# Kernel tuning notes

Hardware: AMD Instinct MI355X
Metric: run time of the kernel (lower is better)

## Reference

```python
import jax, jax.numpy as jnp
import numpy as np

AT_ID = 5       # tokenizer id of '@'
CITSEG_ID = 7   # tokenizer id of 'CITSEG'


def setup_inputs() -> dict:
    key = jax.random.key(0)
    ks = jax.random.split(key, 12)
    B, S, H = 256, 512, 768
    CIT, D, NC = 750, 1518, 6
    s = lambda n: 1.0 / np.sqrt(n)
    return {
        "tokens": jax.random.randint(ks[0], (B, S), 0, 100),
        "hidden_states": jax.random.normal(ks[1], (B, S, H), jnp.float32),
        "proj_w": jax.random.normal(ks[2], (H, CIT), jnp.float32) * s(H),
        "proj_b": jax.random.normal(ks[3], (CIT,), jnp.float32) * 0.02,
        "enc_w": jax.random.normal(ks[4], (CIT, CIT), jnp.float32) * s(CIT),
        "enc_b": jax.random.normal(ks[5], (CIT,), jnp.float32) * 0.02,
        "w1": jax.random.normal(ks[6], (D, 2 * D), jnp.float32) * s(D),
        "b1": jax.random.normal(ks[7], (2 * D,), jnp.float32) * 0.02,
        "w2": jax.random.normal(ks[8], (2 * D, 2 * D), jnp.float32) * s(2 * D),
        "b2": jax.random.normal(ks[9], (2 * D,), jnp.float32) * 0.02,
        "w3": jax.random.normal(ks[10], (2 * D, NC), jnp.float32) * s(2 * D),
        "b3": jax.random.normal(ks[11], (NC,), jnp.float32) * 0.02,
    }


def _forward(tokens, hidden_states, proj_w, proj_b, enc_w, enc_b,
             w1, b1, w2, b2, w3, b3):
    B, S, H = hidden_states.shape
    idx = jnp.arange(S)[None, :]                       # [1,S]
    BIG = S + 1

    # --- ctx_pooler: masked max over tokens outside the [start,end] '@' span ---
    at_mask = tokens == AT_ID                          # [B,S]
    first = jnp.min(jnp.where(at_mask, idx, BIG), axis=1)            # [B]
    second = jnp.min(jnp.where(at_mask & (idx > first[:, None]), idx, BIG), axis=1)
    ge2 = at_mask.sum(axis=1) >= 2
    start = jnp.where(ge2, first, 0)
    end = jnp.where(ge2, second, S)                    # end=S excludes everything
    keep = (idx < start[:, None]) | (idx > end[:, None])             # [B,S]
    neg = jnp.finfo(hidden_states.dtype).min
    pooled = jnp.max(jnp.where(keep[:, :, None], hidden_states, neg), axis=1)  # [B,H]
    pooled = jnp.where(keep.any(axis=1)[:, None], pooled, 0.0)

    # --- CITSEG token gather + projection (zero row if absent) ---
    c_mask = tokens == CITSEG_ID
    c_first = jnp.min(jnp.where(c_mask, idx, BIG), axis=1)           # [B]
    has_c = c_mask.any(axis=1)
    safe_pos = jnp.minimum(c_first, S - 1)
    cit_h = jnp.take_along_axis(hidden_states, safe_pos[:, None, None], axis=1)[:, 0]  # [B,H]
    cit = (cit_h @ proj_w + proj_b) * has_c[:, None].astype(hidden_states.dtype)       # [B,750]

    # --- citseg_encoder (modeled as Linear 750->750) ---
    cit_enc = cit @ enc_w + enc_b

    # --- MLP head ---
    x = jnp.concatenate([pooled, cit_enc], axis=1)     # [B,1518]
    x = jax.nn.relu(x @ w1 + b1)
    x = jax.nn.relu(x @ w2 + b2)
    return x @ w3 + b3                                 # [B,num_class]


def reference(tokens, hidden_states, proj_w, proj_b, enc_w, enc_b,
              w1, b1, w2, b2, w3, b3):
    return _forward(tokens, hidden_states, proj_w, proj_b, enc_w, enc_b,
                    w1, b1, w2, b2, w3, b3)
```

## Files before the change

kernel.cpp:

```cpp
#include <hip/hip_runtime.h>
#include <hip/hip_bf16.h>

typedef __attribute__((ext_vector_type(8))) short bf16x8;
typedef __attribute__((ext_vector_type(4))) float f32x4;
typedef __attribute__((ext_vector_type(2))) float f32x2;
typedef __attribute__((ext_vector_type(4))) unsigned short u16x4;

#define NEGINF (-3.4028234663852886e38f)
#define BIGP (1 << 20)

__device__ __forceinline__ unsigned short f2b(float f) {
    union { float f; unsigned u; } x; x.f = f;
    unsigned r = x.u + 0x7FFFu + ((x.u >> 16) & 1u);
    return (unsigned short)(r >> 16);
}
__device__ __forceinline__ float b2f(unsigned short b) {
    union { unsigned u; float f; } x; x.u = ((unsigned)b) << 16;
    return x.f;
}
__device__ __forceinline__ void load_lds16(const void* g, void* l) {
    __builtin_amdgcn_global_load_lds((const __attribute__((address_space(1))) void*)g,
                                     (__attribute__((address_space(3))) void*)l, 16, 0, 0);
}
__device__ __forceinline__ int swzf(int r) { return (r & 15) ^ (r >> 4); }

#define GEMM_COMPUTE(as, bs)                                                        \
    _Pragma("unroll")                                                               \
    for (int ks = 0; ks < 4; ++ks) {                                                \
        int kc = ks * 4 + rsub;                                                     \
        bf16x8 af[2], bfr[2];                                                       \
        _Pragma("unroll")                                                           \
        for (int mi = 0; mi < 2; ++mi) {                                            \
            int rr = wr * 32 + mi * 16 + c_lin;                                     \
            af[mi] = *(const bf16x8*)((as) + rr * 128 + ((kc ^ c_lin ^ (wr * 2 + mi)) << 3)); \
        }                                                                           \
        _Pragma("unroll")                                                           \
        for (int nj = 0; nj < 2; ++nj) {                                            \
            int rr = wc * 32 + nj * 16 + c_lin;                                     \
            bfr[nj] = *(const bf16x8*)((bs) + rr * 128 + ((kc ^ c_lin ^ (wc * 2 + nj)) << 3)); \
        }                                                                           \
        _Pragma("unroll")                                                           \
        for (int mi = 0; mi < 2; ++mi)                                              \
            _Pragma("unroll")                                                       \
            for (int nj = 0; nj < 2; ++nj)                                          \
                acc[mi][nj] = __builtin_amdgcn_mfma_f32_16x16x32_bf16(              \
                    af[mi], bfr[nj], acc[mi][nj], 0, 0, 0);                         \
    }

__device__ __forceinline__ void wpe_body(const float* __restrict__ proj,
                                         const float* __restrict__ enc,
                                         unsigned short* __restrict__ WpeT,
                                         int bx, int by,
                                         unsigned short* AsB, unsigned short* BsB) {
    const int KR = 750;
    const int tid = threadIdx.x;
    const int wid = tid >> 6, lane = tid & 63;
    const int m0 = by * 64, n0 = bx * 64;
    const int wr = wid >> 1, wc = wid & 1;
    const int c_lin = lane & 15, rsub = lane >> 4;
    const int tn = (tid & 15) * 4, tc = tid >> 4;

    f32x4 acc[2][2];
    const f32x4 zero = {0.f, 0.f, 0.f, 0.f};
#pragma unroll
    for (int mi = 0; mi < 2; ++mi)
#pragma unroll
        for (int nj = 0; nj < 2; ++nj) acc[mi][nj] = zero;

    for (int t = 0; t < 6; ++t) {
        int kt = t << 7;
        float va[4][8];
#pragma unroll
        for (int p = 0; p < 4; ++p) {
            int r = m0 + p * 16 + tc;
#pragma unroll
            for (int e = 0; e < 4; ++e) {
                int d = kt + (tid & 15) * 8 + e * 2;
                int dcl = min(d, KR - 2);
                f32x2 t2 = *(const f32x2*)(proj + (size_t)r * KR + dcl);
                va[p][e * 2]     = (d < KR) ? t2[0] : 0.f;
                va[p][e * 2 + 1] = (d + 1 < KR) ? t2[1] : 0.f;
            }
        }
        f32x4 vb[8];
        int nbl = n0 + tn;
        int n1 = min(nbl, 748), n2 = min(nbl + 2, 748);
#pragma unroll
        for (int p = 0; p < 8; ++p) {
            int kg = min(kt + tc * 8 + p, KR - 1);
            const float* rowp = enc + (size_t)kg * KR;
            f32x2 a = *(const f32x2*)(rowp + n1);
            f32x2 b = *(const f32x2*)(rowp + n2);
            f32x4 tv; tv[0] = a[0]; tv[1] = a[1]; tv[2] = b[0]; tv[3] = b[1];
            vb[p] = tv;
        }
        __syncthreads();
#pragma unroll
        for (int p = 0; p < 4; ++p) {
            int r = p * 16 + tc;
            bf16x8 w;
#pragma unroll
            for (int e = 0; e < 8; ++e) w[e] = (short)f2b(va[p][e]);
            *(bf16x8*)(AsB + r * 128 + (((tid & 15) ^ swzf(r)) << 3)) = w;
        }
#pragma unroll
        for (int q = 0; q < 4; ++q) {
            int row = tn + q;
            bf16x8 w;
#pragma unroll
            for (int p = 0; p < 8; ++p) w[p] = (short)f2b(vb[p][q]);
            *(bf16x8*)(BsB + row * 128 + ((tc ^ swzf(row)) << 3)) = w;
        }
        __syncthreads();
        const unsigned short* as = AsB;
        const unsigned short* bs = BsB;
        GEMM_COMPUTE(as, bs)
    }
#pragma unroll
    for (int mi = 0; mi < 2; ++mi) {
        int hb = m0 + wr * 32 + mi * 16 + rsub * 4;
#pragma unroll
        for (int nj = 0; nj < 2; ++nj) {
            int j = n0 + wc * 32 + nj * 16 + c_lin;
#pragma unroll
            for (int i = 0; i < 4; ++i)
                WpeT[(size_t)j * 768 + hb + i] = f2b(acc[mi][nj][i]);
        }
    }
}

__device__ __forceinline__ void trans32(const float* __restrict__ in, int K, int N,
                                        unsigned short* __restrict__ out, int ldo,
                                        int bx, int by, int tid, float (*tile)[33]) {
    int n0 = bx * 32, k0 = by * 32;
    int tx = tid & 31, ty = tid >> 5;
#pragma unroll
    for (int i = 0; i < 4; ++i) {
        int k = k0 + ty * 4 + i, n = n0 + tx;
        tile[ty * 4 + i][tx] = (k < K && n < N) ? in[(size_t)k * N + n] : 0.f;
    }
    __syncthreads();
    int n = tid >> 3, kc = tid & 7;
    u16x4 o;
#pragma unroll
    for (int q = 0; q < 4; ++q) o[q] = f2b(tile[kc * 4 + q][n]);
    *(u16x4*)(out + (size_t)(n0 + n) * ldo + k0 + kc * 4) = o;
}

__global__ __launch_bounds__(256) void kA_k(
    const int* __restrict__ tokens, const float* __restrict__ hs,
    int* __restrict__ meta, unsigned short* __restrict__ citA,
    const float* __restrict__ proj_w, const float* __restrict__ enc_w,
    const float* __restrict__ proj_b, const float* __restrict__ enc_b,
    unsigned short* __restrict__ WpeT, float* __restrict__ bpe,
    float* __restrict__ part,
    const float* __restrict__ w1, const float* __restrict__ w2,
    unsigned short* __restrict__ w1T, unsigned short* __restrict__ w2T) {
    __shared__ __align__(16) char smem[32768];
    int bid = blockIdx.x, tid = threadIdx.x;
    if (bid < 64) {
        const int S = 512;
        int b = bid * 4 + (tid >> 6), l = tid & 63;
        const int* row = tokens + (size_t)b * S;
        int base = l * 8;
        int toks[8];
#pragma unroll
        for (int i = 0; i < 8; ++i) toks[i] = row[base + i];
        int am = 0, cnt = 0, minAt = BIGP, minC = BIGP;
#pragma unroll
        for (int i = 0; i < 8; ++i) {
            if (toks[i] == 5) { am |= 1 << i; cnt++; if (base + i < minAt) minAt = base + i; }
            if (toks[i] == 7) { if (base + i < minC) minC = base + i; }
        }
        for (int off = 1; off < 64; off <<= 1) {
            minAt = min(minAt, __shfl_xor(minAt, off));
            minC  = min(minC,  __shfl_xor(minC,  off));
            cnt  += __shfl_xor(cnt, off);
        }
        int first = minAt, minAt2 = BIGP;
#pragma unroll
        for (int i = 0; i < 8; ++i)
            if ((am >> i) & 1) { int idx = base + i; if (idx > first && idx < minAt2) minAt2 = idx; }
        for (int off = 1; off < 64; off <<= 1) minAt2 = min(minAt2, __shfl_xor(minAt2, off));
        if (l == 0) {
            int ge2 = (cnt >= 2) ? 1 : 0;
            int start = ge2 ? first : 0;
            int end = ge2 ? minAt2 : S;
            int anyKeep = (ge2 && (start > 0 || end < S - 1)) ? 1 : 0;
            int has_c = (minC < S) ? 1 : 0;
            int cpos = min(minC, S - 1);
            int* m = meta + b * 6;
            m[0] = start; m[1] = end; m[2] = cpos; m[3] = has_c; m[4] = anyKeep; m[5] = 0;
        }
        return;
    }
    if (bid < 320) {
        if (tid >= 192) return;
        int b = bid - 64, lane = tid & 63;
        const int* row = tokens + (size_t)b * 512;
        int minC = BIGP;
#pragma unroll
        for (int c = 0; c < 8; ++c) {
            int tok = row[c * 64 + lane];
            unsigned long long m = __ballot(tok == 7);
            if (minC == BIGP && m) minC = c * 64 + (int)__ffsll(m) - 1;
        }
        int cpos = min(minC, 511);
        f32x4 cv = *(const f32x4*)(hs + ((size_t)b * 512 + cpos) * 768 + tid * 4);
        u16x4 co;
#pragma unroll
        for (int j = 0; j < 4; ++j) co[j] = f2b(cv[j]);
        *(u16x4*)(citA + (size_t)b * 768 + tid * 4) = co;
        return;
    }
    if (bid < 464) {
        int r = bid - 320;
        wpe_body(proj_w, enc_w, WpeT, r % 12, r / 12,
                 (unsigned short*)smem, (unsigned short*)(smem + 16384));
        return;
    }
    if (bid < 467) {
        int j = (bid - 464) * 256 + tid;
        if (j < 750) {
            float a = enc_b[j];
            for (int d = 0; d < 750; ++d) a += proj_b[d] * enc_w[(size_t)d * 750 + j];
            bpe[j] = a;
        }
        return;
    }
    if (bid < 2515) {
        if (tid >= 192) return;
        int pb = bid - 467;
        int b = pb >> 3, ch = pb & 7;
        int lane = tid & 63;
        const int* row = tokens + (size_t)b * 512;
        int first = BIGP, second = BIGP;
#pragma unroll
        for (int c = 0; c < 8; ++c) {
            int tok = row[c * 64 + lane];
            unsigned long long m = __ballot(tok == 5);
            if (m) {
                int base = c * 64;
                if (first == BIGP) {
                    first = base + (int)__ffsll(m) - 1;
                    unsigned long long m2 = m & (m - 1);
                    if (m2) second = base + (int)__ffsll(m2) - 1;
                } else if (second == BIGP) {
                    second = base + (int)__ffsll(m) - 1;
                }
            }
        }
        int start, end;
        if (second < BIGP) { start = first; end = second; }
        else               { start = 0;     end = 512;    }
        f32x4 m = { NEGINF, NEGINF, NEGINF, NEGINF };
        const float* basep = hs + (size_t)b * 512 * 768 + tid * 4;
        int s0 = ch * 64, hi = s0 + 64;
        int e1 = min(start, hi);
        int s2 = max(end + 1, s0);
#pragma unroll 4
        for (int s = s0; s < e1; ++s) {
            f32x4 v = *(const f32x4*)(basep + (size_t)s * 768);
#pragma unroll
            for (int j = 0; j < 4; ++j) m[j] = fmaxf(m[j], v[j]);
        }
#pragma unroll 4
        for (int s = s2; s < hi; ++s) {
            f32x4 v = *(const f32x4*)(basep + (size_t)s * 768);
#pragma unroll
            for (int j = 0; j < 4; ++j) m[j] = fmaxf(m[j], v[j]);
        }
        *(f32x4*)(part + ((size_t)b * 8 + ch) * 768 + tid * 4) = m;
        return;
    }
    if (bid < 7123) {
        int r = bid - 2515;
        trans32(w1, 1518, 3036, w1T, 1536, r % 96, r / 96, tid, (float(*)[33])(void*)smem);
        return;
    }
    {
        int r = bid - 7123;
        trans32(w2, 3036, 3036, w2T, 3072, r % 96, r / 96, tid, (float(*)[33])(void*)smem);
    }
}

__device__ __forceinline__ void g12_body(
    const unsigned short* __restrict__ A, const unsigned short* __restrict__ Bt,
    const float* __restrict__ bpe, const float* __restrict__ encb,
    const int* __restrict__ meta, unsigned short* __restrict__ X,
    int bx, int by, unsigned short* AsB, unsigned short* BsB) {
    const int lda = 768, ldb = 768, ldx = 1536, Nreal = 750;
    const int tid = threadIdx.x;
    const int wid = tid >> 6, lane = tid & 63;
    const int m0 = by * 64, n0 = bx * 64;
    const int wr = wid >> 1, wc = wid & 1;
    const int c_lin = lane & 15, rsub = lane >> 4;

    int aoff[4], boff[4], ldst[4];
#pragma unroll
    for (int i = 0; i < 4; ++i) {
        int r = wid * 16 + i * 4 + rsub;
        int csrc = (c_lin ^ swzf(r)) << 3;
        aoff[i] = (m0 + r) * lda + csrc;
        boff[i] = (n0 + r) * ldb + csrc;
        ldst[i] = (wid * 16 + i * 4) * 128;
    }
    f32x4 acc[2][2];
    const f32x4 zero = {0.f, 0.f, 0.f, 0.f};
#pragma unroll
    for (int mi = 0; mi < 2; ++mi)
#pragma unroll
        for (int nj = 0; nj < 2; ++nj) acc[mi][nj] = zero;

    auto stage = [&](int nb, int kt) {
#pragma unroll
        for (int i = 0; i < 4; ++i) load_lds16(A + aoff[i] + kt, AsB + nb * 8192 + ldst[i]);
#pragma unroll
        for (int i = 0; i < 4; ++i) load_lds16(Bt + boff[i] + kt, BsB + nb * 8192 + ldst[i]);
    };
    const int nt = 6;
    stage(0, 0);
    int cb = 0;
    for (int t = 0; t < nt; ++t) {
        __syncthreads();
        if (t + 1 < nt) stage(cb ^ 1, (t + 1) << 7);
        const unsigned short* as = AsB + cb * 8192;
        const unsigned short* bs = BsB + cb * 8192;
        GEMM_COMPUTE(as, bs)
        cb ^= 1;
    }
#pragma unroll
    for (int mi = 0; mi < 2; ++mi) {
        int rowb = m0 + wr * 32 + mi * 16 + rsub * 4;
#pragma unroll
        for (int nj = 0; nj < 2; ++nj) {
            int col = n0 + wc * 32 + nj * 16 + c_lin;
            float bv = (col < Nreal) ? bpe[col] : 0.f;
            float ev = (col < Nreal) ? encb[col] : 0.f;
#pragma unroll
            for (int i = 0; i < 4; ++i) {
                int row = rowb + i;
                float v = acc[mi][nj][i] + bv;
                v = meta[row * 6 + 3] ? v : ev;
                if (col >= Nreal) v = 0.f;
                X[(size_t)row * ldx + col] = f2b(v);
            }
        }
    }
}

__global__ __launch_bounds__(256, 2) void pack_g12_k(
    const float* __restrict__ part, const int* __restrict__ meta,
    unsigned short* __restrict__ xA,
    const unsigned short* __restrict__ citA, const unsigned short* __restrict__ WpeT,
    const float* __restrict__ bpe, const float* __restrict__ encb) {
    __shared__ __align__(16) unsigned short As[2][8192];
    __shared__ __align__(16) unsigned short Bs[2][8192];
    int bid = blockIdx.x, tid = threadIdx.x;
    if (bid < 256) {
        if (tid >= 192) return;
        int b = bid;
        const float* p = part + (size_t)b * 8 * 768 + tid * 4;
        f32x4 m = *(const f32x4*)p;
#pragma unroll
        for (int ch = 1; ch < 8; ++ch) {
            f32x4 v = *(const f32x4*)(p + (size_t)ch * 768);
#pragma unroll
            for (int j = 0; j < 4; ++j) m[j] = fmaxf(m[j], v[j]);
        }
        if (!meta[b * 6 + 4]) {
            f32x4 z = {0.f, 0.f, 0.f, 0.f};
            m = z;
        }
        u16x4 o;
#pragma unroll
        for (int j = 0; j < 4; ++j) o[j] = f2b(m[j]);
        *(u16x4*)(xA + (size_t)b * 1536 + tid * 4) = o;
        return;
    }
    int r = bid - 256;
    g12_body(citA, WpeT, bpe, encb, meta, xA + 768, r % 12, r / 12, &As[0][0], &Bs[0][0]);
}

template<int EPI>
__global__ __launch_bounds__(256, 2) void gemm_k(
    const unsigned short* __restrict__ A, int lda,
    const unsigned short* __restrict__ Bt, int ldb,
    const float* __restrict__ bias, const int* __restrict__ meta,
    unsigned short* __restrict__ X, int ldx, int Nreal, int Kp) {
    __shared__ __align__(16) unsigned short As[2][8192];
    __shared__ __align__(16) unsigned short Bs[2][8192];
    unsigned short* AsB = &As[0][0];
    unsigned short* BsB = &Bs[0][0];
    const int tid = threadIdx.x;
    const int wid = tid >> 6, lane = tid & 63;
    const int m0 = blockIdx.y * 64, n0 = blockIdx.x * 64;
    const int wr = wid >> 1, wc = wid & 1;
    const int c_lin = lane & 15;
    const int rsub = lane >> 4;

    int aoff[4], boff[4], ldst[4];
#pragma unroll
    for (int i = 0; i < 4; ++i) {
        int r = wid * 16 + i * 4 + rsub;
        int csrc = (c_lin ^ (r & 15)) << 3;
        aoff[i] = (m0 + r) * lda + csrc;
        boff[i] = (n0 + r) * ldb + csrc;
        ldst[i] = (wid * 16 + i * 4) * 128;
    }
    int cswz[4];
#pragma unroll
    for (int ks = 0; ks < 4; ++ks) cswz[ks] = ((ks * 4 + rsub) ^ c_lin) << 3;
    int arow[2], brow[2];
#pragma unroll
    for (int mi = 0; mi < 2; ++mi) arow[mi] = (wr * 32 + mi * 16 + c_lin) * 128;
#pragma unroll
    for (int nj = 0; nj < 2; ++nj) brow[nj] = (wc * 32 + nj * 16 + c_lin) * 128;

    f32x4 acc[2][2];
    const f32x4 zero = {0.f, 0.f, 0.f, 0.f};
#pragma unroll
    for (int mi = 0; mi < 2; ++mi)
#pragma unroll
        for (int nj = 0; nj < 2; ++nj) acc[mi][nj] = zero;

    auto stage = [&](int nb, int kt) {
#pragma unroll
        for (int i = 0; i < 4; ++i) load_lds16(A + aoff[i] + kt, AsB + nb * 8192 + ldst[i]);
#pragma unroll
        for (int i = 0; i < 4; ++i) load_lds16(Bt + boff[i] + kt, BsB + nb * 8192 + ldst[i]);
    };

    const int nt = Kp >> 7;
    stage(0, 0);
    int cb = 0;
    for (int t = 0; t < nt; ++t) {
        __syncthreads();
        if (t + 1 < nt) stage(cb ^ 1, (t + 1) << 7);
        const unsigned short* as = AsB + cb * 8192;
        const unsigned short* bs = BsB + cb * 8192;
#pragma unroll
        for (int ks = 0; ks < 4; ++ks) {
            bf16x8 af[2], bfr[2];
#pragma unroll
            for (int mi = 0; mi < 2; ++mi) af[mi] = *(const bf16x8*)(as + arow[mi] + cswz[ks]);
#pragma unroll
            for (int nj = 0; nj < 2; ++nj) bfr[nj] = *(const bf16x8*)(bs + brow[nj] + cswz[ks]);
#pragma unroll
            for (int mi = 0; mi < 2; ++mi)
#pragma unroll
                for (int nj = 0; nj < 2; ++nj)
                    acc[mi][nj] = __builtin_amdgcn_mfma_f32_16x16x32_bf16(
                        af[mi], bfr[nj], acc[mi][nj], 0, 0, 0);
        }
        cb ^= 1;
    }
#pragma unroll
    for (int mi = 0; mi < 2; ++mi) {
        int rowb = m0 + wr * 32 + mi * 16 + rsub * 4;
#pragma unroll
        for (int nj = 0; nj < 2; ++nj) {
            int col = n0 + wc * 32 + nj * 16 + c_lin;
            float bv = (col < Nreal) ? bias[col] : 0.f;
#pragma unroll
            for (int i = 0; i < 4; ++i) {
                float v = acc[mi][nj][i] + bv;
                if (EPI == 2) v = fmaxf(v, 0.f);
                if (col >= Nreal) v = 0.f;
                X[(size_t)(rowb + i) * ldx + col] = f2b(v);
            }
        }
    }
}

__global__ __launch_bounds__(256) void out_k(const unsigned short* __restrict__ x2,
                                             const float* __restrict__ w3,
                                             const float* __restrict__ b3,
                                             float* __restrict__ out) {
    int b = blockIdx.x, t = threadIdx.x;
    int wid = t >> 6, lane = t & 63;
    float s[6] = {0.f, 0.f, 0.f, 0.f, 0.f, 0.f};
    const unsigned short* xr = x2 + (size_t)b * 3072;
    for (int k = t; k < 3036; k += 256) {
        float x = b2f(xr[k]);
#pragma unroll
        for (int j = 0; j < 6; ++j) s[j] += x * w3[(size_t)k * 6 + j];
    }
#pragma unroll
    for (int j = 0; j < 6; ++j)
        for (int off = 1; off < 64; off <<= 1) s[j] += __shfl_xor(s[j], off);
    __shared__ float red[4][6];
    if (lane == 0) {
#pragma unroll
        for (int j = 0; j < 6; ++j) red[wid][j] = s[j];
    }
    __syncthreads();
    if (t < 6) out[b * 6 + t] = red[0][t] + red[1][t] + red[2][t] + red[3][t] + b3[t];
}

extern "C" void kernel_launch(void* const* d_in, const int* in_sizes, int n_in,
                              void* d_out, int out_size, void* d_ws, size_t ws_size,
                              hipStream_t stream) {
    const int*   tokens = (const int*)d_in[0];
    const float* hs     = (const float*)d_in[1];
    const float* proj_w = (const float*)d_in[2];
    const float* proj_b = (const float*)d_in[3];
    const float* enc_w  = (const float*)d_in[4];
    const float* enc_b  = (const float*)d_in[5];
    const float* w1 = (const float*)d_in[6];
    const float* b1 = (const float*)d_in[7];
    const float* w2 = (const float*)d_in[8];
    const float* b2 = (const float*)d_in[9];
    const float* w3 = (const float*)d_in[10];
    const float* b3 = (const float*)d_in[11];
    float* out = (float*)d_out;

    char* ws = (char*)d_ws;
    size_t off = 0;
    auto alloc = [&](size_t bytes) {
        void* p = ws + off;
        off = (off + bytes + 255) & ~(size_t)255;
        return p;
    };
    int* meta            = (int*)alloc(256 * 6 * sizeof(int));
    float* part          = (float*)alloc((size_t)256 * 8 * 768 * sizeof(float));
    unsigned short* xA   = (unsigned short*)alloc((size_t)256 * 1536 * 2);
    unsigned short* citA = (unsigned short*)alloc((size_t)256 * 768 * 2);
    unsigned short* x1   = (unsigned short*)alloc((size_t)256 * 3072 * 2);
    unsigned short* x2   = (unsigned short*)alloc((size_t)256 * 3072 * 2);
    unsigned short* WpeT = (unsigned short*)alloc((size_t)768 * 768 * 2);
    float* bpe           = (float*)alloc(768 * sizeof(float));
    unsigned short* w1T  = (unsigned short*)alloc((size_t)3072 * 1536 * 2);
    unsigned short* w2T  = (unsigned short*)alloc((size_t)3072 * 3072 * 2);

    kA_k<<<16339, 256, 0, stream>>>(tokens, hs, meta, citA, proj_w, enc_w,
                                    proj_b, enc_b, WpeT, bpe, part, w1, w2, w1T, w2T);
    pack_g12_k<<<304, 256, 0, stream>>>(part, meta, xA, citA, WpeT, bpe, enc_b);
    gemm_k<2><<<dim3(48, 4), 256, 0, stream>>>(xA, 1536, w1T, 1536, b1, meta,
                                               x1, 3072, 3036, 1536);
    gemm_k<2><<<dim3(48, 4), 256, 0, stream>>>(x1, 3072, w2T, 3072, b2, meta,
                                               x2, 3072, 3036, 3072);
    out_k<<<256, 256, 0, stream>>>(x2, w3, b3, out);
}
```

Baseline: 164.4 us.

## Split prep kernel and triple-buffer GEMM K-loop with vmcnt-based waits

```diff
diff --git a/kernel.cpp b/kernel.cpp
--- a/kernel.cpp
+++ b/kernel.cpp
@@ -129,33 +129,12 @@
     }
 }
 
-__device__ __forceinline__ void trans32(const float* __restrict__ in, int K, int N,
-                                        unsigned short* __restrict__ out, int ldo,
-                                        int bx, int by, int tid, float (*tile)[33]) {
-    int n0 = bx * 32, k0 = by * 32;
-    int tx = tid & 31, ty = tid >> 5;
-#pragma unroll
-    for (int i = 0; i < 4; ++i) {
-        int k = k0 + ty * 4 + i, n = n0 + tx;
-        tile[ty * 4 + i][tx] = (k < K && n < N) ? in[(size_t)k * N + n] : 0.f;
-    }
-    __syncthreads();
-    int n = tid >> 3, kc = tid & 7;
-    u16x4 o;
-#pragma unroll
-    for (int q = 0; q < 4; ++q) o[q] = f2b(tile[kc * 4 + q][n]);
-    *(u16x4*)(out + (size_t)(n0 + n) * ldo + k0 + kc * 4) = o;
-}
-
-__global__ __launch_bounds__(256) void kA_k(
+__global__ __launch_bounds__(256) void k1_prep_k(
     const int* __restrict__ tokens, const float* __restrict__ hs,
     int* __restrict__ meta, unsigned short* __restrict__ citA,
     const float* __restrict__ proj_w, const float* __restrict__ enc_w,
     const float* __restrict__ proj_b, const float* __restrict__ enc_b,
-    unsigned short* __restrict__ WpeT, float* __restrict__ bpe,
-    float* __restrict__ part,
-    const float* __restrict__ w1, const float* __restrict__ w2,
-    unsigned short* __restrict__ w1T, unsigned short* __restrict__ w2T) {
+    unsigned short* __restrict__ WpeT, float* __restrict__ bpe) {
     __shared__ __align__(16) char smem[32768];
     int bid = blockIdx.x, tid = threadIdx.x;
     if (bid < 64) {
@@ -219,40 +198,45 @@
                  (unsigned short*)smem, (unsigned short*)(smem + 16384));
         return;
     }
-    if (bid < 467) {
+    {
         int j = (bid - 464) * 256 + tid;
         if (j < 750) {
             float a = enc_b[j];
             for (int d = 0; d < 750; ++d) a += proj_b[d] * enc_w[(size_t)d * 750 + j];
             bpe[j] = a;
         }
-        return;
-    }
-    if (bid < 2515) {
+    }
+}
+
+__device__ __forceinline__ void trans32(const float* __restrict__ in, int K, int N,
+                                        unsigned short* __restrict__ out, int ldo,
+                                        int bx, int by, int tid, float (*tile)[33]) {
+    int n0 = bx * 32, k0 = by * 32;
+    int tx = tid & 31, ty = tid >> 5;
+#pragma unroll
+    for (int i = 0; i < 4; ++i) {
+        int k = k0 + ty * 4 + i, n = n0 + tx;
+        tile[ty * 4 + i][tx] = (k < K && n < N) ? in[(size_t)k * N + n] : 0.f;
+    }
+    __syncthreads();
+    int n = tid >> 3, kc = tid & 7;
+    u16x4 o;
+#pragma unroll
+    for (int q = 0; q < 4; ++q) o[q] = f2b(tile[kc * 4 + q][n]);
+    *(u16x4*)(out + (size_t)(n0 + n) * ldo + k0 + kc * 4) = o;
+}
+
+__global__ __launch_bounds__(256) void pool_trans_k(
+    const float* __restrict__ hs, const int* __restrict__ meta,
+    float* __restrict__ part,
+    const float* __restrict__ w1, const float* __restrict__ w2,
+    unsigned short* __restrict__ w1T, unsigned short* __restrict__ w2T) {
+    __shared__ float tile[32][33];
+    int bid = blockIdx.x, tid = threadIdx.x;
+    if (bid < 2048) {
         if (tid >= 192) return;
-        int pb = bid - 467;
-        int b = pb >> 3, ch = pb & 7;
-        int lane = tid & 63;
-        const int* row = tokens + (size_t)b * 512;
-        int first = BIGP, second = BIGP;
-#pragma unroll
-        for (int c = 0; c < 8; ++c) {
-            int tok = row[c * 64 + lane];
-            unsigned long long m = __ballot(tok == 5);
-            if (m) {
-                int base = c * 64;
-                if (first == BIGP) {
-                    first = base + (int)__ffsll(m) - 1;
-                    unsigned long long m2 = m & (m - 1);
-                    if (m2) second = base + (int)__ffsll(m2) - 1;
-                } else if (second == BIGP) {
-                    second = base + (int)__ffsll(m) - 1;
-                }
-            }
-        }
-        int start, end;
-        if (second < BIGP) { start = first; end = second; }
-        else               { start = 0;     end = 512;    }
+        int b = bid >> 3, ch = bid & 7;
+        int start = meta[b * 6 + 0], end = meta[b * 6 + 1];
         f32x4 m = { NEGINF, NEGINF, NEGINF, NEGINF };
         const float* basep = hs + (size_t)b * 512 * 768 + tid * 4;
         int s0 = ch * 64, hi = s0 + 64;
@@ -273,15 +257,10 @@
         *(f32x4*)(part + ((size_t)b * 8 + ch) * 768 + tid * 4) = m;
         return;
     }
-    if (bid < 7123) {
-        int r = bid - 2515;
-        trans32(w1, 1518, 3036, w1T, 1536, r % 96, r / 96, tid, (float(*)[33])(void*)smem);
-        return;
-    }
-    {
-        int r = bid - 7123;
-        trans32(w2, 3036, 3036, w2T, 3072, r % 96, r / 96, tid, (float(*)[33])(void*)smem);
-    }
+    int r = bid - 2048;
+    if (r < 4608) { trans32(w1, 1518, 3036, w1T, 1536, r % 96, r / 96, tid, tile); return; }
+    r -= 4608;
+    trans32(w2, 3036, 3036, w2T, 3072, r % 96, r / 96, tid, tile);
 }
 
 __device__ __forceinline__ void g12_body(
@@ -382,16 +361,13 @@
     g12_body(citA, WpeT, bpe, encb, meta, xA + 768, r % 12, r / 12, &As[0][0], &Bs[0][0]);
 }
 
-template<int EPI>
-__global__ __launch_bounds__(256, 2) void gemm_k(
+__global__ __launch_bounds__(256, 1) void gemm3_k(
     const unsigned short* __restrict__ A, int lda,
     const unsigned short* __restrict__ Bt, int ldb,
-    const float* __restrict__ bias, const int* __restrict__ meta,
+    const float* __restrict__ bias,
     unsigned short* __restrict__ X, int ldx, int Nreal, int Kp) {
-    __shared__ __align__(16) unsigned short As[2][8192];
-    __shared__ __align__(16) unsigned short Bs[2][8192];
-    unsigned short* AsB = &As[0][0];
-    unsigned short* BsB = &Bs[0][0];
+    __shared__ __align__(16) unsigned short As[3][8192];
+    __shared__ __align__(16) unsigned short Bs[3][8192];
     const int tid = threadIdx.x;
     const int wid = tid >> 6, lane = tid & 63;
     const int m0 = blockIdx.y * 64, n0 = blockIdx.x * 64;
@@ -426,19 +402,22 @@
 
     auto stage = [&](int nb, int kt) {
 #pragma unroll
-        for (int i = 0; i < 4; ++i) load_lds16(A + aoff[i] + kt, AsB + nb * 8192 + ldst[i]);
-#pragma unroll
-        for (int i = 0; i < 4; ++i) load_lds16(Bt + boff[i] + kt, BsB + nb * 8192 + ldst[i]);
+        for (int i = 0; i < 4; ++i) load_lds16(A + aoff[i] + kt, &As[0][0] + nb * 8192 + ldst[i]);
+#pragma unroll
+        for (int i = 0; i < 4; ++i) load_lds16(Bt + boff[i] + kt, &Bs[0][0] + nb * 8192 + ldst[i]);
     };
 
     const int nt = Kp >> 7;
     stage(0, 0);
-    int cb = 0;
+    stage(1, 128);
     for (int t = 0; t < nt; ++t) {
-        __syncthreads();
-        if (t + 1 < nt) stage(cb ^ 1, (t + 1) << 7);
-        const unsigned short* as = AsB + cb * 8192;
-        const unsigned short* bs = BsB + cb * 8192;
+        if (t + 1 < nt) asm volatile("s_waitcnt vmcnt(8)" ::: "memory");
+        else            asm volatile("s_waitcnt vmcnt(0)" ::: "memory");
+        __builtin_amdgcn_s_barrier();
+        __builtin_amdgcn_sched_barrier(0);
+        if (t + 2 < nt) stage((t + 2) % 3, (t + 2) << 7);
+        const unsigned short* as = &As[0][0] + (t % 3) * 8192;
+        const unsigned short* bs = &Bs[0][0] + (t % 3) * 8192;
 #pragma unroll
         for (int ks = 0; ks < 4; ++ks) {
             bf16x8 af[2], bfr[2];
@@ -453,7 +432,6 @@
                     acc[mi][nj] = __builtin_amdgcn_mfma_f32_16x16x32_bf16(
                         af[mi], bfr[nj], acc[mi][nj], 0, 0, 0);
         }
-        cb ^= 1;
     }
 #pragma unroll
     for (int mi = 0; mi < 2; ++mi) {
@@ -464,8 +442,7 @@
             float bv = (col < Nreal) ? bias[col] : 0.f;
 #pragma unroll
             for (int i = 0; i < 4; ++i) {
-                float v = acc[mi][nj][i] + bv;
-                if (EPI == 2) v = fmaxf(v, 0.f);
+                float v = fmaxf(acc[mi][nj][i] + bv, 0.f);
                 if (col >= Nreal) v = 0.f;
                 X[(size_t)(rowb + i) * ldx + col] = f2b(v);
             }
@@ -533,12 +510,11 @@
     unsigned short* w1T  = (unsigned short*)alloc((size_t)3072 * 1536 * 2);
     unsigned short* w2T  = (unsigned short*)alloc((size_t)3072 * 3072 * 2);
 
-    kA_k<<<16339, 256, 0, stream>>>(tokens, hs, meta, citA, proj_w, enc_w,
-                                    proj_b, enc_b, WpeT, bpe, part, w1, w2, w1T, w2T);
+    k1_prep_k<<<467, 256, 0, stream>>>(tokens, hs, meta, citA, proj_w, enc_w,
+                                       proj_b, enc_b, WpeT, bpe);
+    pool_trans_k<<<15872, 256, 0, stream>>>(hs, meta, part, w1, w2, w1T, w2T);
     pack_g12_k<<<304, 256, 0, stream>>>(part, meta, xA, citA, WpeT, bpe, enc_b);
-    gemm_k<2><<<dim3(48, 4), 256, 0, stream>>>(xA, 1536, w1T, 1536, b1, meta,
-                                               x1, 3072, 3036, 1536);
-    gemm_k<2><<<dim3(48, 4), 256, 0, stream>>>(x1, 3072, w2T, 3072, b2, meta,
-                                               x2, 3072, 3036, 3072);
+    gemm3_k<<<dim3(48, 4), 256, 0, stream>>>(xA, 1536, w1T, 1536, b1, x1, 3072, 3036, 1536);
+    gemm3_k<<<dim3(48, 4), 256, 0, stream>>>(x1, 3072, w2T, 3072, b2, x2, 3072, 3036, 3072);
     out_k<<<256, 256, 0, stream>>>(x2, w3, b3, out);
 }
```

After: 187.3 us. +13.9%, slower.
